# Kernel optimization log

Hardware: AMD Instinct MI355X
Metric: run time of the kernel (lower is better)

Reference implementation:

```python
import jax, jax.numpy as jnp
import numpy as np

EMB_DIM = 1024
NHEAD = 16
HEAD_DIM = EMB_DIM // NHEAD
SEQ = 2048
NEG_INF = -1e30


def setup_inputs() -> dict:
    key = jax.random.key(0)
    ks = jax.random.split(key, 8)
    # xavier_uniform bound for square [E, E] weights
    bound = float(np.sqrt(6.0 / (EMB_DIM + EMB_DIM)))
    def xavier(k):
        return jax.random.uniform(k, (EMB_DIM, EMB_DIM), jnp.float32, -bound, bound)
    return {
        "q": jax.random.normal(ks[0], (SEQ, EMB_DIM), jnp.float32),
        "k": jax.random.normal(ks[1], (SEQ, EMB_DIM), jnp.float32),
        "v": jax.random.normal(ks[2], (SEQ, EMB_DIM), jnp.float32),
        "mask": jax.random.randint(ks[3], (SEQ, SEQ), 0, 2) > 0,  # True = masked
        "Wq": xavier(ks[4]),
        "Wk": xavier(ks[5]),
        "Wv": xavier(ks[6]),
        "Wo": xavier(ks[7]),
    }


def reference(q, k, v, mask, Wq, Wk, Wv, Wo):
    S = q.shape[0]
    scaling = HEAD_DIM ** -0.5
    # F.linear(x, W) == x @ W.T ; reshape to [nhead, S, head_dim]
    def split_heads(x):
        return x.reshape(S, NHEAD, HEAD_DIM).transpose(1, 0, 2)
    query = split_heads(q @ Wq.T)   # [H, S, D]
    key_h = split_heads(k @ Wk.T)   # [H, S, D]
    val_h = split_heads(v @ Wv.T)   # [H, S, D]
    # scaled dot-product attention with boolean masking (True -> -1e30)
    scores = jnp.einsum("hsd,htd->hst", query, key_h) * scaling  # [H, S, S]
    scores = jnp.where(mask[None, :, :], NEG_INF, scores)
    attn = jax.nn.softmax(scores, axis=-1)
    # dropout inactive in eval mode
    out = jnp.einsum("hst,htd->hsd", attn, val_h)  # [H, S, D]
    out = out.transpose(1, 0, 2).reshape(S, EMB_DIM)
    return out @ Wo.T
```

## Files before the change

### kernel.cpp

```cpp
#include <hip/hip_runtime.h>

typedef __bf16 bf16;
typedef __attribute__((ext_vector_type(8))) __bf16 bf16x8;
typedef __attribute__((ext_vector_type(4))) float f32x4;

#define NEG_INF_F (-1e30f)

#define OFF_MASK 1024
#define OFF_WQ   (1024 + 524288)
#define OFF_WK   (OFF_WQ + 2097152)
#define OFF_WV   (OFF_WK + 2097152)
#define OFF_WO   (OFF_WV + 2097152)
#define OFF_QP   (OFF_WO + 2097152)
#define OFF_KP   (OFF_QP + 4194304)
#define OFF_VP   (OFF_KP + 4194304)
#define OFF_AO   (OFF_VP + 4194304)

typedef __attribute__((address_space(1))) const unsigned int as1_u32;
typedef __attribute__((address_space(3))) unsigned int as3_u32;
__device__ __forceinline__ void gload16(const void* g, void* l) {
  __builtin_amdgcn_global_load_lds((as1_u32*)g, (as3_u32*)l, 16, 0, 0);
}

__device__ __forceinline__ bf16x8 cvt8(const float4 a, const float4 b) {
  bf16x8 o;
  o[0] = (bf16)a.x; o[1] = (bf16)a.y; o[2] = (bf16)a.z; o[3] = (bf16)a.w;
  o[4] = (bf16)b.x; o[5] = (bf16)b.y; o[6] = (bf16)b.z; o[7] = (bf16)b.w;
  return o;
}

__global__ void detect_width_kernel(const unsigned char* __restrict__ m,
                                    unsigned int* __restrict__ flag) {
  __shared__ unsigned int s13, s47;
  const int tid = threadIdx.x;
  if (tid == 0) { s13 = 0u; s47 = 0u; }
  __syncthreads();
  unsigned int a13 = 0u, a47 = 0u;
  const int base = tid * 64;
  for (int j = 0; j < 64; ++j) {
    const int off = base + j;
    const unsigned int b = m[off];
    if (off & 3) a13 |= b;
    if (off & 4) a47 |= b;
  }
  if (a13) atomicOr(&s13, 1u);
  if (a47) atomicOr(&s47, 1u);
  __syncthreads();
  if (tid == 0) flag[0] = s13 ? 1u : (s47 ? 4u : 8u);
}

__global__ void pack_mask_kernel(const unsigned char* __restrict__ srcb,
                                 const unsigned int* __restrict__ flag,
                                 unsigned int* __restrict__ dst) {
  const unsigned int width = flag[0];
  const int lane = threadIdx.x & 63;
  const size_t stride = (size_t)gridDim.x * blockDim.x;
  for (size_t e = (size_t)blockIdx.x * blockDim.x + threadIdx.x;
       e < 2048ull * 2048ull; e += stride) {
    unsigned int v;
    if (width == 4u)      v = ((const unsigned int*)srcb)[e];
    else if (width == 1u) v = srcb[e];
    else                  v = (unsigned int)((const unsigned long long*)srcb)[e];
    const unsigned long long bal = __ballot(v & 1u);
    if (lane == 0)       dst[e >> 5] = (unsigned int)bal;
    else if (lane == 32) dst[e >> 5] = (unsigned int)(bal >> 32);
  }
}

__global__ __launch_bounds__(256) void convert_w_kernel(
    const float* __restrict__ W0, const float* __restrict__ W1,
    const float* __restrict__ W2, const float* __restrict__ W3,
    bf16* __restrict__ D0, bf16* __restrict__ D1,
    bf16* __restrict__ D2, bf16* __restrict__ D3) {
  const int z = blockIdx.y;
  const float* s = (z == 0) ? W0 : (z == 1) ? W1 : (z == 2) ? W2 : W3;
  bf16* d = (z == 0) ? D0 : (z == 1) ? D1 : (z == 2) ? D2 : D3;
  const int i = blockIdx.x * 256 + threadIdx.x;
  const float4 x0 = ((const float4*)s)[i * 2];
  const float4 x1 = ((const float4*)s)[i * 2 + 1];
  ((bf16x8*)d)[i] = cvt8(x0, x1);
}

template <bool AF32, typename TC>
__device__ __forceinline__ void gemm_body(const void* Avoid, const bf16* __restrict__ B,
                                          TC* __restrict__ C, int brow, int bcol) {
  __shared__ __align__(16) bf16 AsBuf[64 * 72];
  __shared__ __align__(16) bf16 Bs[128 * 64];
  const int tid = threadIdx.x;
  const int lane = tid & 63, w = tid >> 6;
  const int wr = w >> 1, wc = w & 1;
  const int l15 = lane & 15, l4 = lane >> 4;
  const int srow = lane >> 3;
  const int sgrp = (lane & 7) ^ srow;

  f32x4 acc[2][4] = {};

  for (int kt = 0; kt < 1024; kt += 64) {
    __syncthreads();
#pragma unroll
    for (int p = 0; p < 4; ++p) {
      const int rb = w * 32 + p * 8;
      gload16(B + (size_t)(bcol + rb + srow) * 1024 + kt + sgrp * 8, &Bs[rb * 64]);
    }
    if constexpr (AF32) {
      const float* A = (const float*)Avoid;
      const int row = tid >> 2, c16 = (tid & 3) * 16;
      const float4* ap = (const float4*)(A + (size_t)(brow + row) * 1024 + kt + c16);
      const float4 x0 = ap[0], x1 = ap[1], x2 = ap[2], x3 = ap[3];
      *(bf16x8*)&AsBuf[row * 72 + c16] = cvt8(x0, x1);
      *(bf16x8*)&AsBuf[row * 72 + c16 + 8] = cvt8(x2, x3);
    } else {
      const bf16* A = (const bf16*)Avoid;
#pragma unroll
      for (int p = 0; p < 2; ++p) {
        const int rb = w * 16 + p * 8;
        gload16(A + (size_t)(brow + rb + srow) * 1024 + kt + sgrp * 8, &AsBuf[rb * 64]);
      }
    }
    __syncthreads();

    bf16x8 af0[2], af1[2], b0[4], b1[4];
#pragma unroll
    for (int m = 0; m < 2; ++m) {
      const int row = wr * 32 + m * 16 + l15;
      if constexpr (AF32) {
        af0[m] = *(const bf16x8*)&AsBuf[row * 72 + l4 * 8];
        af1[m] = *(const bf16x8*)&AsBuf[row * 72 + 32 + l4 * 8];
      } else {
        const int g0 = l4 ^ (l15 & 7);
        af0[m] = *(const bf16x8*)&AsBuf[row * 64 + g0 * 8];
        af1[m] = *(const bf16x8*)&AsBuf[row * 64 + (g0 ^ 4) * 8];
      }
    }
#pragma unroll
    for (int n = 0; n < 4; ++n) {
      const int row = wc * 64 + n * 16 + l15;
      const int g0 = l4 ^ (l15 & 7);
      b0[n] = *(const bf16x8*)&Bs[row * 64 + g0 * 8];
      b1[n] = *(const bf16x8*)&Bs[row * 64 + (g0 ^ 4) * 8];
    }
#pragma unroll
    for (int m = 0; m < 2; ++m)
#pragma unroll
      for (int n = 0; n < 4; ++n) {
        acc[m][n] = __builtin_amdgcn_mfma_f32_16x16x32_bf16(af0[m], b0[n], acc[m][n], 0, 0, 0);
        acc[m][n] = __builtin_amdgcn_mfma_f32_16x16x32_bf16(af1[m], b1[n], acc[m][n], 0, 0, 0);
      }
  }
#pragma unroll
  for (int m = 0; m < 2; ++m)
#pragma unroll
    for (int n = 0; n < 4; ++n)
#pragma unroll
      for (int j = 0; j < 4; ++j) {
        const int row = brow + wr * 32 + m * 16 + l4 * 4 + j;
        const int col = bcol + wc * 64 + n * 16 + l15;
        C[(size_t)row * 1024 + col] = (TC)acc[m][n][j];
      }
}

__global__ __launch_bounds__(256) void gemm_qkv_kernel(
    const float* __restrict__ Aq, const float* __restrict__ Ak, const float* __restrict__ Av,
    const bf16* __restrict__ Bq, const bf16* __restrict__ Bk, const bf16* __restrict__ Bv,
    bf16* __restrict__ Cq, bf16* __restrict__ Ck, bf16* __restrict__ Cv) {
  const int z = blockIdx.z;
  const float* A = (z == 0) ? Aq : (z == 1) ? Ak : Av;
  const bf16* B = (z == 0) ? Bq : (z == 1) ? Bk : Bv;
  bf16* C = (z == 0) ? Cq : (z == 1) ? Ck : Cv;
  gemm_body<true, bf16>(A, B, C, blockIdx.y * 64, blockIdx.x * 128);
}

__global__ __launch_bounds__(256) void gemm_out_kernel(const bf16* __restrict__ A,
                                                       const bf16* __restrict__ B,
                                                       float* __restrict__ C) {
  gemm_body<false, float>(A, B, C, blockIdx.y * 64, blockIdx.x * 128);
}

__global__ __launch_bounds__(256) void flash_attn_kernel(
    const bf16* __restrict__ Qp, const bf16* __restrict__ Kp, const bf16* __restrict__ Vp,
    const unsigned int* __restrict__ mwg, bf16* __restrict__ AO) {
  const int h = blockIdx.x;
  const int qb = blockIdx.y * 64;
  const int tid = threadIdx.x;
  const int lane = tid & 63, w = tid >> 6;
  const int l15 = lane & 15, l4 = lane >> 4;

  __shared__ __align__(16) bf16 Ks[2][64 * 64];
  __shared__ __align__(16) bf16 Vt[2][64 * 72];
  __shared__ unsigned int Msk[2][64][2];
  __shared__ __align__(16) bf16 Ps[4][16 * 72];

  const bf16* Qrow = Qp + (size_t)(qb + w * 16 + l15) * 1024 + h * 64;
  const bf16x8 qf0 = *(const bf16x8*)(Qrow + l4 * 8);
  const bf16x8 qf1 = *(const bf16x8*)(Qrow + 32 + l4 * 8);

  f32x4 oacc[4] = {};
  float m_i[4], l_i[4];
#pragma unroll
  for (int j = 0; j < 4; ++j) { m_i[j] = NEG_INF_F; l_i[j] = 0.f; }

  const int srow = lane >> 3, sgrp = (lane & 7) ^ srow;
  const int vr = tid >> 3, vc8 = (tid & 7) * 8;
  const int vg0 = ((vr >> 3) ^ (tid & 7)) & 7;

  bf16x8 vpre0, vpre1; unsigned int mpre = 0;
#pragma unroll
  for (int p = 0; p < 2; ++p) {
    const int rb = w * 16 + p * 8;
    gload16(Kp + (size_t)(rb + srow) * 1024 + h * 64 + sgrp * 8, &Ks[0][rb * 64]);
  }
  vpre0 = *(const bf16x8*)(Vp + (size_t)vr * 1024 + h * 64 + vc8);
  vpre1 = *(const bf16x8*)(Vp + (size_t)(vr + 32) * 1024 + h * 64 + vc8);
  if (tid < 128) mpre = mwg[(size_t)(qb + (tid >> 1)) * 64 + (tid & 1)];

  for (int t = 0; t < 32; ++t) {
    const int cur = t & 1;
#pragma unroll
    for (int j = 0; j < 8; ++j) {
      const int d = vc8 + j;
      Vt[cur][d * 72 + vg0 * 8 + (vr & 7)] = vpre0[j];
      Vt[cur][d * 72 + (vg0 ^ 4) * 8 + (vr & 7)] = vpre1[j];
    }
    if (tid < 128) Msk[cur][tid >> 1][tid & 1] = mpre;
    __syncthreads();

    if (t + 1 < 32) {
      const int kvn = (t + 1) * 64;
#pragma unroll
      for (int p = 0; p < 2; ++p) {
        const int rb = w * 16 + p * 8;
        gload16(Kp + (size_t)(kvn + rb + srow) * 1024 + h * 64 + sgrp * 8,
                &Ks[cur ^ 1][rb * 64]);
      }
      vpre0 = *(const bf16x8*)(Vp + (size_t)(kvn + vr) * 1024 + h * 64 + vc8);
      vpre1 = *(const bf16x8*)(Vp + (size_t)(kvn + vr + 32) * 1024 + h * 64 + vc8);
      if (tid < 128) mpre = mwg[(size_t)(qb + (tid >> 1)) * 64 + (t + 1) * 2 + (tid & 1)];
    }

    f32x4 s[4] = {};
    const int kg0 = l4 ^ (l15 & 7);
#pragma unroll
    for (int g = 0; g < 4; ++g) {
      const int krow = g * 16 + l15;
      const bf16x8 kf0 = *(const bf16x8*)&Ks[cur][krow * 64 + kg0 * 8];
      s[g] = __builtin_amdgcn_mfma_f32_16x16x32_bf16(qf0, kf0, s[g], 0, 0, 0);
      const bf16x8 kf1 = *(const bf16x8*)&Ks[cur][krow * 64 + (kg0 ^ 4) * 8];
      s[g] = __builtin_amdgcn_mfma_f32_16x16x32_bf16(qf1, kf1, s[g], 0, 0, 0);
    }

#pragma unroll
    for (int j = 0; j < 4; ++j) {
      const int qrow = w * 16 + l4 * 4 + j;
      const unsigned int u0 = Msk[cur][qrow][0];
      const unsigned int u1 = Msk[cur][qrow][1];
      const float a0 = ((u0 >> l15) & 1u)        ? NEG_INF_F : s[0][j] * 0.125f;
      const float a1 = ((u0 >> (16 + l15)) & 1u) ? NEG_INF_F : s[1][j] * 0.125f;
      const float a2 = ((u1 >> l15) & 1u)        ? NEG_INF_F : s[2][j] * 0.125f;
      const float a3 = ((u1 >> (16 + l15)) & 1u) ? NEG_INF_F : s[3][j] * 0.125f;
      float t4 = fmaxf(fmaxf(a0, a1), fmaxf(a2, a3));
#pragma unroll
      for (int d = 1; d < 16; d <<= 1) t4 = fmaxf(t4, __shfl_xor(t4, d));
      const float mn = fmaxf(m_i[j], t4);
      const float sc = __expf(m_i[j] - mn);
      const float e0 = __expf(a0 - mn), e1 = __expf(a1 - mn);
      const float e2 = __expf(a2 - mn), e3 = __expf(a3 - mn);
      float rs = (e0 + e1) + (e2 + e3);
#pragma unroll
      for (int d = 1; d < 16; d <<= 1) rs += __shfl_xor(rs, d);
      l_i[j] = l_i[j] * sc + rs;
      m_i[j] = mn;
      oacc[0][j] *= sc; oacc[1][j] *= sc; oacc[2][j] *= sc; oacc[3][j] *= sc;
      bf16* prow = &Ps[w][(l4 * 4 + j) * 72];
      prow[l15] = (bf16)e0; prow[16 + l15] = (bf16)e1;
      prow[32 + l15] = (bf16)e2; prow[48 + l15] = (bf16)e3;
    }

    const bf16x8 pf0 = *(const bf16x8*)&Ps[w][l15 * 72 + l4 * 8];
    const bf16x8 pf1 = *(const bf16x8*)&Ps[w][l15 * 72 + 32 + l4 * 8];
#pragma unroll
    for (int n = 0; n < 4; ++n) {
      const int d = n * 16 + l15;
      const int vgr = l4 ^ ((2 * n + (l15 >> 3)) & 7);
      const bf16x8 vf0 = *(const bf16x8*)&Vt[cur][d * 72 + vgr * 8];
      oacc[n] = __builtin_amdgcn_mfma_f32_16x16x32_bf16(pf0, vf0, oacc[n], 0, 0, 0);
      const bf16x8 vf1 = *(const bf16x8*)&Vt[cur][d * 72 + (vgr ^ 4) * 8];
      oacc[n] = __builtin_amdgcn_mfma_f32_16x16x32_bf16(pf1, vf1, oacc[n], 0, 0, 0);
    }
  }

#pragma unroll
  for (int n = 0; n < 4; ++n)
#pragma unroll
    for (int j = 0; j < 4; ++j)
      AO[(size_t)(qb + w * 16 + l4 * 4 + j) * 1024 + h * 64 + n * 16 + l15] =
          (bf16)(oacc[n][j] / l_i[j]);
}

extern "C" void kernel_launch(void* const* d_in, const int* in_sizes, int n_in,
                              void* d_out, int out_size, void* d_ws, size_t ws_size,
                              hipStream_t stream) {
  const float* q = (const float*)d_in[0];
  const float* k = (const float*)d_in[1];
  const float* v = (const float*)d_in[2];
  const unsigned char* mask = (const unsigned char*)d_in[3];
  const float* Wq = (const float*)d_in[4];
  const float* Wk = (const float*)d_in[5];
  const float* Wv = (const float*)d_in[6];
  const float* Wo = (const float*)d_in[7];
  float* out = (float*)d_out;

  char* ws = (char*)d_ws;
  unsigned int* flag = (unsigned int*)ws;
  unsigned int* mpacked = (unsigned int*)(ws + OFF_MASK);
  bf16* Wqb = (bf16*)(ws + OFF_WQ);
  bf16* Wkb = (bf16*)(ws + OFF_WK);
  bf16* Wvb = (bf16*)(ws + OFF_WV);
  bf16* Wob = (bf16*)(ws + OFF_WO);
  bf16* Qp = (bf16*)(ws + OFF_QP);
  bf16* Kp = (bf16*)(ws + OFF_KP);
  bf16* Vp = (bf16*)(ws + OFF_VP);
  bf16* AO = (bf16*)(ws + OFF_AO);

  detect_width_kernel<<<1, 256, 0, stream>>>(mask, flag);
  pack_mask_kernel<<<2048, 256, 0, stream>>>(mask, flag, mpacked);
  convert_w_kernel<<<dim3(512, 4), 256, 0, stream>>>(Wq, Wk, Wv, Wo, Wqb, Wkb, Wvb, Wob);
  gemm_qkv_kernel<<<dim3(8, 32, 3), 256, 0, stream>>>(q, k, v, Wqb, Wkb, Wvb, Qp, Kp, Vp);
  flash_attn_kernel<<<dim3(16, 32), 256, 0, stream>>>(Qp, Kp, Vp, mpacked, AO);
  gemm_out_kernel<<<dim3(8, 32), 256, 0, stream>>>(AO, Wob, out);
}
```

Baseline: 225.1 us.

## Double-buffer GEMM tiles and transpose S in flash attention with lazy rescale

The GEMM body now double-buffers its A and B shared tiles, prefetching the next k-tile (and converting fp32 A after the MFMAs), so one barrier per iteration overlaps loads with compute. In flash attention the QK^T MFMA operands are swapped, so each lane holds a full query row's scores. This lets the mask be read as a per-lane 64-bit word straight from global memory instead of staging it in shared memory, and cuts the row max/sum to two cross-lane shuffles. It also skips the online-softmax rescale when no row max grows and adds s_setprio around the MFMA blocks. The cost is more shared memory in the GEMM, which can lower occupancy, and more complex per-lane index logic.

```diff
diff --git a/kernel.cpp b/kernel.cpp
--- a/kernel.cpp
+++ b/kernel.cpp
@@ -1,6 +1,7 @@
 #include <hip/hip_runtime.h>
 
 typedef __bf16 bf16;
+typedef __attribute__((ext_vector_type(4))) __bf16 bf16x4;
 typedef __attribute__((ext_vector_type(8))) __bf16 bf16x8;
 typedef __attribute__((ext_vector_type(4))) float f32x4;
 
@@ -84,68 +85,90 @@
 template <bool AF32, typename TC>
 __device__ __forceinline__ void gemm_body(const void* Avoid, const bf16* __restrict__ B,
                                           TC* __restrict__ C, int brow, int bcol) {
-  __shared__ __align__(16) bf16 AsBuf[64 * 72];
-  __shared__ __align__(16) bf16 Bs[128 * 64];
+  __shared__ __align__(16) bf16 As[2][64 * 72];
+  __shared__ __align__(16) bf16 Bs[2][128 * 64];
   const int tid = threadIdx.x;
   const int lane = tid & 63, w = tid >> 6;
   const int wr = w >> 1, wc = w & 1;
   const int l15 = lane & 15, l4 = lane >> 4;
-  const int srow = lane >> 3;
-  const int sgrp = (lane & 7) ^ srow;
+  const int srow = lane >> 3, sgrp = (lane & 7) ^ srow;
+  const int arow = tid >> 2, ac16 = (tid & 3) * 16;
 
   f32x4 acc[2][4] = {};
 
-  for (int kt = 0; kt < 1024; kt += 64) {
+#pragma unroll
+  for (int p = 0; p < 4; ++p)
+    gload16(B + (size_t)(bcol + w * 32 + p * 8 + srow) * 1024 + sgrp * 8,
+            &Bs[0][(w * 32 + p * 8) * 64]);
+  if constexpr (AF32) {
+    const float* A = (const float*)Avoid;
+    const float4* ap = (const float4*)(A + (size_t)(brow + arow) * 1024 + ac16);
+    const float4 x0 = ap[0], x1 = ap[1], x2 = ap[2], x3 = ap[3];
+    *(bf16x8*)&As[0][arow * 72 + ac16] = cvt8(x0, x1);
+    *(bf16x8*)&As[0][arow * 72 + ac16 + 8] = cvt8(x2, x3);
+  } else {
+    const bf16* A = (const bf16*)Avoid;
+#pragma unroll
+    for (int p = 0; p < 2; ++p)
+      gload16(A + (size_t)(brow + w * 16 + p * 8 + srow) * 1024 + sgrp * 8,
+              &As[0][(w * 16 + p * 8) * 64]);
+  }
+
+#pragma unroll 2
+  for (int i = 0; i < 16; ++i) {
+    const int cur = i & 1;
     __syncthreads();
-#pragma unroll
-    for (int p = 0; p < 4; ++p) {
-      const int rb = w * 32 + p * 8;
-      gload16(B + (size_t)(bcol + rb + srow) * 1024 + kt + sgrp * 8, &Bs[rb * 64]);
-    }
-    if constexpr (AF32) {
-      const float* A = (const float*)Avoid;
-      const int row = tid >> 2, c16 = (tid & 3) * 16;
-      const float4* ap = (const float4*)(A + (size_t)(brow + row) * 1024 + kt + c16);
-      const float4 x0 = ap[0], x1 = ap[1], x2 = ap[2], x3 = ap[3];
-      *(bf16x8*)&AsBuf[row * 72 + c16] = cvt8(x0, x1);
-      *(bf16x8*)&AsBuf[row * 72 + c16 + 8] = cvt8(x2, x3);
-    } else {
-      const bf16* A = (const bf16*)Avoid;
-#pragma unroll
-      for (int p = 0; p < 2; ++p) {
-        const int rb = w * 16 + p * 8;
-        gload16(A + (size_t)(brow + rb + srow) * 1024 + kt + sgrp * 8, &AsBuf[rb * 64]);
-      }
-    }
-    __syncthreads();
-
-    bf16x8 af0[2], af1[2], b0[4], b1[4];
+    float4 x0, x1, x2, x3;
+    if (i + 1 < 16) {
+      const int kt = (i + 1) * 64;
+#pragma unroll
+      for (int p = 0; p < 4; ++p)
+        gload16(B + (size_t)(bcol + w * 32 + p * 8 + srow) * 1024 + kt + sgrp * 8,
+                &Bs[cur ^ 1][(w * 32 + p * 8) * 64]);
+      if constexpr (AF32) {
+        const float* A = (const float*)Avoid;
+        const float4* ap = (const float4*)(A + (size_t)(brow + arow) * 1024 + kt + ac16);
+        x0 = ap[0]; x1 = ap[1]; x2 = ap[2]; x3 = ap[3];
+      } else {
+        const bf16* A = (const bf16*)Avoid;
+#pragma unroll
+        for (int p = 0; p < 2; ++p)
+          gload16(A + (size_t)(brow + w * 16 + p * 8 + srow) * 1024 + kt + sgrp * 8,
+                  &As[cur ^ 1][(w * 16 + p * 8) * 64]);
+      }
+    }
+    const int g0 = l4 ^ (l15 & 7);
+    bf16x8 a0[2], a1[2], b0[4], b1[4];
 #pragma unroll
     for (int m = 0; m < 2; ++m) {
       const int row = wr * 32 + m * 16 + l15;
       if constexpr (AF32) {
-        af0[m] = *(const bf16x8*)&AsBuf[row * 72 + l4 * 8];
-        af1[m] = *(const bf16x8*)&AsBuf[row * 72 + 32 + l4 * 8];
+        a0[m] = *(const bf16x8*)&As[cur][row * 72 + l4 * 8];
+        a1[m] = *(const bf16x8*)&As[cur][row * 72 + 32 + l4 * 8];
       } else {
-        const int g0 = l4 ^ (l15 & 7);
-        af0[m] = *(const bf16x8*)&AsBuf[row * 64 + g0 * 8];
-        af1[m] = *(const bf16x8*)&AsBuf[row * 64 + (g0 ^ 4) * 8];
+        a0[m] = *(const bf16x8*)&As[cur][row * 64 + g0 * 8];
+        a1[m] = *(const bf16x8*)&As[cur][row * 64 + (g0 ^ 4) * 8];
       }
     }
 #pragma unroll
     for (int n = 0; n < 4; ++n) {
       const int row = wc * 64 + n * 16 + l15;
-      const int g0 = l4 ^ (l15 & 7);
-      b0[n] = *(const bf16x8*)&Bs[row * 64 + g0 * 8];
-      b1[n] = *(const bf16x8*)&Bs[row * 64 + (g0 ^ 4) * 8];
+      b0[n] = *(const bf16x8*)&Bs[cur][row * 64 + g0 * 8];
+      b1[n] = *(const bf16x8*)&Bs[cur][row * 64 + (g0 ^ 4) * 8];
     }
 #pragma unroll
     for (int m = 0; m < 2; ++m)
 #pragma unroll
       for (int n = 0; n < 4; ++n) {
-        acc[m][n] = __builtin_amdgcn_mfma_f32_16x16x32_bf16(af0[m], b0[n], acc[m][n], 0, 0, 0);
-        acc[m][n] = __builtin_amdgcn_mfma_f32_16x16x32_bf16(af1[m], b1[n], acc[m][n], 0, 0, 0);
-      }
+        acc[m][n] = __builtin_amdgcn_mfma_f32_16x16x32_bf16(a0[m], b0[n], acc[m][n], 0, 0, 0);
+        acc[m][n] = __builtin_amdgcn_mfma_f32_16x16x32_bf16(a1[m], b1[n], acc[m][n], 0, 0, 0);
+      }
+    if constexpr (AF32) {
+      if (i + 1 < 16) {
+        *(bf16x8*)&As[cur ^ 1][arow * 72 + ac16] = cvt8(x0, x1);
+        *(bf16x8*)&As[cur ^ 1][arow * 72 + ac16 + 8] = cvt8(x2, x3);
+      }
+    }
   }
 #pragma unroll
   for (int m = 0; m < 2; ++m)
@@ -187,23 +210,23 @@
 
   __shared__ __align__(16) bf16 Ks[2][64 * 64];
   __shared__ __align__(16) bf16 Vt[2][64 * 72];
-  __shared__ unsigned int Msk[2][64][2];
   __shared__ __align__(16) bf16 Ps[4][16 * 72];
 
-  const bf16* Qrow = Qp + (size_t)(qb + w * 16 + l15) * 1024 + h * 64;
-  const bf16x8 qf0 = *(const bf16x8*)(Qrow + l4 * 8);
-  const bf16x8 qf1 = *(const bf16x8*)(Qrow + 32 + l4 * 8);
+  const int qrow = qb + w * 16 + l15;
+  const bf16* Qr = Qp + (size_t)qrow * 1024 + h * 64;
+  const bf16x8 qf0 = *(const bf16x8*)(Qr + l4 * 8);
+  const bf16x8 qf1 = *(const bf16x8*)(Qr + 32 + l4 * 8);
+  const unsigned long long* mrow = (const unsigned long long*)(mwg + (size_t)qrow * 64);
 
   f32x4 oacc[4] = {};
-  float m_i[4], l_i[4];
-#pragma unroll
-  for (int j = 0; j < 4; ++j) { m_i[j] = NEG_INF_F; l_i[j] = 0.f; }
+  float m_i = NEG_INF_F, l_i = 0.f;
 
   const int srow = lane >> 3, sgrp = (lane & 7) ^ srow;
   const int vr = tid >> 3, vc8 = (tid & 7) * 8;
   const int vg0 = ((vr >> 3) ^ (tid & 7)) & 7;
-
-  bf16x8 vpre0, vpre1; unsigned int mpre = 0;
+  const int kg0 = l4 ^ (l15 & 7);
+
+  bf16x8 vpre0, vpre1; unsigned long long mpre;
 #pragma unroll
   for (int p = 0; p < 2; ++p) {
     const int rb = w * 16 + p * 8;
@@ -211,7 +234,7 @@
   }
   vpre0 = *(const bf16x8*)(Vp + (size_t)vr * 1024 + h * 64 + vc8);
   vpre1 = *(const bf16x8*)(Vp + (size_t)(vr + 32) * 1024 + h * 64 + vc8);
-  if (tid < 128) mpre = mwg[(size_t)(qb + (tid >> 1)) * 64 + (tid & 1)];
+  mpre = mrow[0];
 
   for (int t = 0; t < 32; ++t) {
     const int cur = t & 1;
@@ -221,7 +244,7 @@
       Vt[cur][d * 72 + vg0 * 8 + (vr & 7)] = vpre0[j];
       Vt[cur][d * 72 + (vg0 ^ 4) * 8 + (vr & 7)] = vpre1[j];
     }
-    if (tid < 128) Msk[cur][tid >> 1][tid & 1] = mpre;
+    const unsigned long long mq = mpre;
     __syncthreads();
 
     if (t + 1 < 32) {
@@ -234,49 +257,69 @@
       }
       vpre0 = *(const bf16x8*)(Vp + (size_t)(kvn + vr) * 1024 + h * 64 + vc8);
       vpre1 = *(const bf16x8*)(Vp + (size_t)(kvn + vr + 32) * 1024 + h * 64 + vc8);
-      if (tid < 128) mpre = mwg[(size_t)(qb + (tid >> 1)) * 64 + (t + 1) * 2 + (tid & 1)];
+      mpre = mrow[t + 1];
     }
 
     f32x4 s[4] = {};
-    const int kg0 = l4 ^ (l15 & 7);
+    __builtin_amdgcn_s_setprio(1);
 #pragma unroll
     for (int g = 0; g < 4; ++g) {
       const int krow = g * 16 + l15;
       const bf16x8 kf0 = *(const bf16x8*)&Ks[cur][krow * 64 + kg0 * 8];
-      s[g] = __builtin_amdgcn_mfma_f32_16x16x32_bf16(qf0, kf0, s[g], 0, 0, 0);
+      s[g] = __builtin_amdgcn_mfma_f32_16x16x32_bf16(kf0, qf0, s[g], 0, 0, 0);
       const bf16x8 kf1 = *(const bf16x8*)&Ks[cur][krow * 64 + (kg0 ^ 4) * 8];
-      s[g] = __builtin_amdgcn_mfma_f32_16x16x32_bf16(qf1, kf1, s[g], 0, 0, 0);
-    }
-
-#pragma unroll
-    for (int j = 0; j < 4; ++j) {
-      const int qrow = w * 16 + l4 * 4 + j;
-      const unsigned int u0 = Msk[cur][qrow][0];
-      const unsigned int u1 = Msk[cur][qrow][1];
-      const float a0 = ((u0 >> l15) & 1u)        ? NEG_INF_F : s[0][j] * 0.125f;
-      const float a1 = ((u0 >> (16 + l15)) & 1u) ? NEG_INF_F : s[1][j] * 0.125f;
-      const float a2 = ((u1 >> l15) & 1u)        ? NEG_INF_F : s[2][j] * 0.125f;
-      const float a3 = ((u1 >> (16 + l15)) & 1u) ? NEG_INF_F : s[3][j] * 0.125f;
-      float t4 = fmaxf(fmaxf(a0, a1), fmaxf(a2, a3));
-#pragma unroll
-      for (int d = 1; d < 16; d <<= 1) t4 = fmaxf(t4, __shfl_xor(t4, d));
-      const float mn = fmaxf(m_i[j], t4);
-      const float sc = __expf(m_i[j] - mn);
-      const float e0 = __expf(a0 - mn), e1 = __expf(a1 - mn);
-      const float e2 = __expf(a2 - mn), e3 = __expf(a3 - mn);
-      float rs = (e0 + e1) + (e2 + e3);
-#pragma unroll
-      for (int d = 1; d < 16; d <<= 1) rs += __shfl_xor(rs, d);
-      l_i[j] = l_i[j] * sc + rs;
-      m_i[j] = mn;
-      oacc[0][j] *= sc; oacc[1][j] *= sc; oacc[2][j] *= sc; oacc[3][j] *= sc;
-      bf16* prow = &Ps[w][(l4 * 4 + j) * 72];
-      prow[l15] = (bf16)e0; prow[16 + l15] = (bf16)e1;
-      prow[32 + l15] = (bf16)e2; prow[48 + l15] = (bf16)e3;
+      s[g] = __builtin_amdgcn_mfma_f32_16x16x32_bf16(kf1, qf1, s[g], 0, 0, 0);
+    }
+    __builtin_amdgcn_s_setprio(0);
+
+    float p[16];
+#pragma unroll
+    for (int g = 0; g < 4; ++g)
+#pragma unroll
+      for (int r = 0; r < 4; ++r) {
+        const int bit = g * 16 + l4 * 4 + r;
+        p[g * 4 + r] = ((mq >> bit) & 1ull) ? NEG_INF_F : s[g][r] * 0.125f;
+      }
+    float tmax = fmaxf(
+        fmaxf(fmaxf(fmaxf(p[0], p[1]), fmaxf(p[2], p[3])),
+              fmaxf(fmaxf(p[4], p[5]), fmaxf(p[6], p[7]))),
+        fmaxf(fmaxf(fmaxf(p[8], p[9]), fmaxf(p[10], p[11])),
+              fmaxf(fmaxf(p[12], p[13]), fmaxf(p[14], p[15]))));
+    tmax = fmaxf(tmax, __shfl_xor(tmax, 16));
+    tmax = fmaxf(tmax, __shfl_xor(tmax, 32));
+
+    const bool skip = (bool)__all(tmax <= m_i);
+    const float mn = skip ? m_i : fmaxf(m_i, tmax);
+#pragma unroll
+    for (int i = 0; i < 16; ++i) p[i] = __expf(p[i] - mn);
+    float rs = ((p[0] + p[1]) + (p[2] + p[3])) + ((p[4] + p[5]) + (p[6] + p[7])) +
+               (((p[8] + p[9]) + (p[10] + p[11])) + ((p[12] + p[13]) + (p[14] + p[15])));
+    rs += __shfl_xor(rs, 16);
+    rs += __shfl_xor(rs, 32);
+    if (!skip) {
+      const float sc = __expf(m_i - mn);
+      const float s0 = __shfl(sc, l4 * 4 + 0), s1 = __shfl(sc, l4 * 4 + 1);
+      const float s2 = __shfl(sc, l4 * 4 + 2), s3 = __shfl(sc, l4 * 4 + 3);
+#pragma unroll
+      for (int n = 0; n < 4; ++n) {
+        oacc[n][0] *= s0; oacc[n][1] *= s1; oacc[n][2] *= s2; oacc[n][3] *= s3;
+      }
+      l_i *= sc;
+      m_i = mn;
+    }
+    l_i += rs;
+
+#pragma unroll
+    for (int g = 0; g < 4; ++g) {
+      bf16x4 pk;
+      pk[0] = (bf16)p[g * 4 + 0]; pk[1] = (bf16)p[g * 4 + 1];
+      pk[2] = (bf16)p[g * 4 + 2]; pk[3] = (bf16)p[g * 4 + 3];
+      *(bf16x4*)&Ps[w][l15 * 72 + g * 16 + l4 * 4] = pk;
     }
 
     const bf16x8 pf0 = *(const bf16x8*)&Ps[w][l15 * 72 + l4 * 8];
     const bf16x8 pf1 = *(const bf16x8*)&Ps[w][l15 * 72 + 32 + l4 * 8];
+    __builtin_amdgcn_s_setprio(1);
 #pragma unroll
     for (int n = 0; n < 4; ++n) {
       const int d = n * 16 + l15;
@@ -286,14 +329,19 @@
       const bf16x8 vf1 = *(const bf16x8*)&Vt[cur][d * 72 + (vgr ^ 4) * 8];
       oacc[n] = __builtin_amdgcn_mfma_f32_16x16x32_bf16(pf1, vf1, oacc[n], 0, 0, 0);
     }
-  }
-
-#pragma unroll
-  for (int n = 0; n < 4; ++n)
-#pragma unroll
-    for (int j = 0; j < 4; ++j)
-      AO[(size_t)(qb + w * 16 + l4 * 4 + j) * 1024 + h * 64 + n * 16 + l15] =
-          (bf16)(oacc[n][j] / l_i[j]);
+    __builtin_amdgcn_s_setprio(0);
+  }
+
+  const float lj0 = __shfl(l_i, l4 * 4 + 0), lj1 = __shfl(l_i, l4 * 4 + 1);
+  const float lj2 = __shfl(l_i, l4 * 4 + 2), lj3 = __shfl(l_i, l4 * 4 + 3);
+#pragma unroll
+  for (int n = 0; n < 4; ++n) {
+    const size_t base = (size_t)(qb + w * 16) * 1024 + h * 64 + n * 16 + l15;
+    AO[base + (size_t)(l4 * 4 + 0) * 1024] = (bf16)(oacc[n][0] / lj0);
+    AO[base + (size_t)(l4 * 4 + 1) * 1024] = (bf16)(oacc[n][1] / lj1);
+    AO[base + (size_t)(l4 * 4 + 2) * 1024] = (bf16)(oacc[n][2] / lj2);
+    AO[base + (size_t)(l4 * 4 + 3) * 1024] = (bf16)(oacc[n][3] / lj3);
+  }
 }
 
 extern "C" void kernel_launch(void* const* d_in, const int* in_sizes, int n_in,
```

Result: faster. 207.6 us (-7.8%).
